# Optimization experiments

Hardware: AMD Instinct MI355X
Metric: run time of the kernel (lower is better)

Reference implementation:

```python
import jax, jax.numpy as jnp
import numpy as np

NUM_HEADS = 32
HEAD_DIM = 128
NUM_KV_HEADS = 8
SCALE = HEAD_DIM ** -0.5
BS = 2
SEQ_LEN = 2048


def setup_inputs() -> dict:
    key = jax.random.key(0)
    kq, kk, kv = jax.random.split(key, 3)
    q = jax.random.normal(kq, (BS * SEQ_LEN, NUM_HEADS * HEAD_DIM), dtype=jnp.float32)
    k = jax.random.normal(kk, (BS * SEQ_LEN, NUM_KV_HEADS * HEAD_DIM), dtype=jnp.float32)
    v = jax.random.normal(kv, (BS * SEQ_LEN, NUM_KV_HEADS * HEAD_DIM), dtype=jnp.float32)
    return {"q": q, "k": k, "v": v, "bs": BS, "seq_len": SEQ_LEN}


def reference(q, k, v, bs, seq_len):
    # Training-path: causal GQA attention (F.scaled_dot_product_attention, is_causal=True)
    qh = q.reshape(bs, seq_len, NUM_HEADS, HEAD_DIM)        # [b, s, h, d]
    kh = k.reshape(bs, seq_len, NUM_KV_HEADS, HEAD_DIM)     # [b, s, hk, d]
    vh = v.reshape(bs, seq_len, NUM_KV_HEADS, HEAD_DIM)
    rep = NUM_HEADS // NUM_KV_HEADS
    kh = jnp.repeat(kh, rep, axis=2)                         # [b, s, h, d]
    vh = jnp.repeat(vh, rep, axis=2)
    # scores [b, h, q, k]
    scores = jnp.einsum("bqhd,bkhd->bhqk", qh, kh) * SCALE
    causal = jnp.tril(jnp.ones((seq_len, seq_len), dtype=bool))
    scores = jnp.where(causal[None, None], scores, jnp.finfo(scores.dtype).min)
    probs = jax.nn.softmax(scores, axis=-1)
    o = jnp.einsum("bhqk,bkhd->bqhd", probs, vh)             # [b, q, h, d]
    return o.reshape(bs * seq_len, NUM_HEADS * HEAD_DIM)
```

## Files before the change

kernel.cpp:

```cpp
#include <hip/hip_runtime.h>

#define NUM_HEADS 32
#define HEAD_DIM 128
#define NUM_KV_HEADS 8
#define SEQ 2048
#define BATCH 2
#define BQ 128

typedef __attribute__((ext_vector_type(8))) short bf16x8;
typedef __attribute__((ext_vector_type(16))) float f32x16;
typedef __attribute__((ext_vector_type(4))) unsigned u32x4;

__device__ __forceinline__ short f2bf(float f) {
    unsigned u = __float_as_uint(f);
    u += 0x7fffu + ((u >> 16) & 1u);
    return (short)(u >> 16);
}
__device__ __forceinline__ unsigned pack2r(float a, float b) {
    unsigned ua = __float_as_uint(a) + 0x8000u;
    unsigned ub = __float_as_uint(b) + 0x8000u;
    return __builtin_amdgcn_perm(ub, ua, 0x07060302);
}
__device__ __forceinline__ float fexp2(float x) { return __builtin_amdgcn_exp2f(x); }

__global__ __launch_bounds__(256)
void conv_kv(const float* __restrict__ kg, const float* __restrict__ vg,
             short* __restrict__ kb, short* __restrict__ vt) {
    const int bid = blockIdx.x, tid = threadIdx.x;
    __shared__ float T[32][132];
    if (bid < 1024) {
        const float SL = 0.08838834764831845f * 1.4426950408889634f;
        int kvt = bid & 63, hk = (bid >> 6) & 7, b = bid >> 9;
#pragma unroll
        for (int i = 0; i < 4; ++i) {
            int slot = i * 256 + tid, row = slot >> 5, col = (slot & 31) * 4;
            float4 v = *(const float4*)(kg + ((size_t)(b * SEQ + kvt * 32 + row) * NUM_KV_HEADS + hk)
                                              * HEAD_DIM + col);
            *(float4*)&T[row][col] = v;
        }
        __syncthreads();
        short* dst = kb + (size_t)(b * NUM_KV_HEADS + hk) * SEQ * HEAD_DIM;
#pragma unroll
        for (int cc = 0; cc < 2; ++cc) {
            int c = tid * 2 + cc;
            int s = c >> 6, lane = c & 63, l32 = lane & 31, half = lane >> 5;
            float4 t0 = *(const float4*)&T[l32][s * 16 + half * 8];
            float4 t1 = *(const float4*)&T[l32][s * 16 + half * 8 + 4];
            bf16x8 o = { f2bf(t0.x * SL), f2bf(t0.y * SL), f2bf(t0.z * SL), f2bf(t0.w * SL),
                         f2bf(t1.x * SL), f2bf(t1.y * SL), f2bf(t1.z * SL), f2bf(t1.w * SL) };
            *(bf16x8*)(dst + ((size_t)(kvt * 8 + s) * 64 + lane) * 8) = o;
        }
    } else {
        int bidx = bid - 1024;
        int kvc = bidx & 63, hk = (bidx >> 6) & 7, b = bidx >> 9;
#pragma unroll
        for (int i = 0; i < 4; ++i) {
            int slot = i * 256 + tid, row = slot >> 5, col = (slot & 31) * 4;
            float4 v = *(const float4*)(vg + ((size_t)(b * SEQ + kvc * 32 + row) * NUM_KV_HEADS + hk)
                                              * HEAD_DIM + col);
            *(float4*)&T[row][col] = v;
        }
        __syncthreads();
        short* dst = vt + (size_t)(b * NUM_KV_HEADS + hk) * SEQ * HEAD_DIM;
#pragma unroll
        for (int cc = 0; cc < 2; ++cc) {
            int c = tid * 2 + cc;
            int chunk = c >> 6;
            int lane = c & 63, l32 = lane & 31, half = lane >> 5;
            int dtile = chunk >> 1, kk = chunk & 1;
            bf16x8 o;
#pragma unroll
            for (int j = 0; j < 8; ++j) o[j] = f2bf(T[kk * 16 + half * 8 + j][dtile * 32 + l32]);
            *(bf16x8*)(dst + ((size_t)(kvc * 8 + chunk) * 64 + lane) * 8) = o;
        }
    }
}

template<bool MASK>
__device__ __forceinline__ void kv_step(const short* __restrict__ Ks,
                                        const short* __restrict__ Vs,
                                        const bf16x8 (&qf)[8], f32x16 (&o)[4],
                                        float& rls, int l32, int half, int lane) {
    f32x16 s4;
#pragma unroll
    for (int r = 0; r < 16; ++r) s4[r] = 0.f;
#pragma unroll
    for (int h2 = 0; h2 < 2; ++h2) {
        bf16x8 kf[4];
#pragma unroll
        for (int s = 0; s < 4; ++s)
            kf[s] = *(const bf16x8*)(Ks + ((h2 * 4 + s) << 9) + lane * 8);
#pragma unroll
        for (int s = 0; s < 4; ++s)
            s4 = __builtin_amdgcn_mfma_f32_32x32x16_bf16(kf[s], qf[h2 * 4 + s], s4, 0, 0, 0);
    }

    if (MASK) {
#pragma unroll
        for (int r = 0; r < 16; ++r) {
            int klocal = (r & 3) + 8 * (r >> 2) + 4 * half;
            s4[r] = (klocal <= l32) ? s4[r] : -1e30f;
        }
    }

#pragma unroll
    for (int r = 0; r < 16; ++r) s4[r] = fexp2(s4[r]);

    {
        float t0 = (s4[0] + s4[1]) + (s4[2] + s4[3]);
        float t1 = (s4[4] + s4[5]) + (s4[6] + s4[7]);
        float t2 = (s4[8] + s4[9]) + (s4[10] + s4[11]);
        float t3 = (s4[12] + s4[13]) + (s4[14] + s4[15]);
        rls += (t0 + t1) + (t2 + t3);
    }

    unsigned p0 = pack2r(s4[0],  s4[1]);
    unsigned p1 = pack2r(s4[2],  s4[3]);
    unsigned p2 = pack2r(s4[4],  s4[5]);
    unsigned p3 = pack2r(s4[6],  s4[7]);
    unsigned p4 = pack2r(s4[8],  s4[9]);
    unsigned p5 = pack2r(s4[10], s4[11]);
    unsigned p6 = pack2r(s4[12], s4[13]);
    unsigned p7 = pack2r(s4[14], s4[15]);
    unsigned t0 = half ? p0 : p2;
    unsigned t1 = half ? p1 : p3;
    unsigned t2 = half ? p4 : p6;
    unsigned t3 = half ? p5 : p7;
    unsigned u0 = (unsigned)__shfl_xor((int)t0, 32);
    unsigned u1 = (unsigned)__shfl_xor((int)t1, 32);
    unsigned u2 = (unsigned)__shfl_xor((int)t2, 32);
    unsigned u3 = (unsigned)__shfl_xor((int)t3, 32);
    u32x4 w0 = { half ? u0 : p0, half ? u1 : p1, half ? p2 : u0, half ? p3 : u1 };
    u32x4 w1 = { half ? u2 : p4, half ? u3 : p5, half ? p6 : u2, half ? p7 : u3 };
    bf16x8 pf0 = __builtin_bit_cast(bf16x8, w0);
    bf16x8 pf1 = __builtin_bit_cast(bf16x8, w1);

#pragma unroll
    for (int h2 = 0; h2 < 2; ++h2) {
        bf16x8 vf[4];
#pragma unroll
        for (int c = 0; c < 4; ++c)
            vf[c] = *(const bf16x8*)(Vs + ((h2 * 4 + c) << 9) + lane * 8);
#pragma unroll
        for (int c = 0; c < 4; ++c) {
            int cg = h2 * 4 + c;
            o[cg >> 1] = __builtin_amdgcn_mfma_f32_32x32x16_bf16(
                vf[c], (cg & 1) ? pf1 : pf0, o[cg >> 1], 0, 0, 0);
        }
    }
}

__global__ __launch_bounds__(256, 3)
void fattn_kernel(const float* __restrict__ qg, const short* __restrict__ kb,
                  const short* __restrict__ vt, float* __restrict__ outg) {
    __shared__ short sh[2][8192];

    const int tid  = threadIdx.x;
    const int wave = tid >> 6;
    const int lane = tid & 63;
    const int l32  = lane & 31;
    const int half = lane >> 5;

    const int bid  = (int)blockIdx.x;
    const int hk   = bid & 7;
    const int rest = bid >> 3;
    const int b    = rest & 1;
    const int hj   = (rest >> 1) & 3;
    const int qt   = 15 - (rest >> 3);
    const int h    = hk * 4 + hj;

    const int q0w = qt * BQ + wave * 32;

    bf16x8 qf[8];
    {
        const float* qp = qg + (size_t)(b * SEQ + q0w + l32) * (NUM_HEADS * HEAD_DIM)
                             + h * HEAD_DIM + half * 8;
#pragma unroll
        for (int s = 0; s < 8; ++s) {
            float4 a = *(const float4*)(qp + s * 16);
            float4 c = *(const float4*)(qp + s * 16 + 4);
            bf16x8 f = { f2bf(a.x), f2bf(a.y), f2bf(a.z), f2bf(a.w),
                         f2bf(c.x), f2bf(c.y), f2bf(c.z), f2bf(c.w) };
            qf[s] = f;
        }
    }

    const short* kreg = kb + (size_t)(b * NUM_KV_HEADS + hk) * SEQ * HEAD_DIM;
    const short* vreg = vt + (size_t)(b * NUM_KV_HEADS + hk) * SEQ * HEAD_DIM;

    f32x16 o[4];
#pragma unroll
    for (int dt = 0; dt < 4; ++dt)
#pragma unroll
        for (int r = 0; r < 16; ++r) o[dt][r] = 0.f;
    float rls = 0.f;

    const int nblk = 4 * qt + 4;
    const int nfw  = 4 * qt + wave;

#define STAGE(ktn, bf_)                                                           \
    {                                                                             \
        const short* ksrc_ = kreg + ((size_t)(ktn) << 12) + lane * 8;             \
        const short* vsrc_ = vreg + ((size_t)(ktn) << 12) + lane * 8;             \
        _Pragma("unroll")                                                         \
        for (int i_ = 0; i_ < 4; ++i_) {                                          \
            int ch_ = wave * 4 + i_;                                              \
            const short* g_ = (ch_ < 8) ? (ksrc_ + (ch_ << 9))                    \
                                        : (vsrc_ + ((ch_ - 8) << 9));             \
            __builtin_amdgcn_global_load_lds(                                     \
                (const __attribute__((address_space(1))) void*)g_,                \
                (__attribute__((address_space(3))) void*)&sh[bf_][ch_ << 9],      \
                16, 0, 0);                                                        \
        }                                                                         \
    }

    STAGE(0, 0);
    __syncthreads();

    int cur = 0;
    for (int kt = 0; kt < nblk; ++kt) {
        if (kt + 1 < nblk) STAGE(kt + 1, cur ^ 1);
        if (kt < nfw)
            kv_step<false>(&sh[cur][0], &sh[cur][4096], qf, o, rls, l32, half, lane);
        else if (kt == nfw)
            kv_step<true>(&sh[cur][0], &sh[cur][4096], qf, o, rls, l32, half, lane);
        __syncthreads();
        cur ^= 1;
    }
#undef STAGE

    const float rl = rls + __shfl_xor(rls, 32);
    const float inv = 1.0f / rl;

    float* op = outg + (size_t)(b * SEQ + q0w + l32) * (NUM_HEADS * HEAD_DIM) + h * HEAD_DIM;
#pragma unroll
    for (int dt = 0; dt < 4; ++dt)
#pragma unroll
        for (int blk = 0; blk < 4; ++blk) {
            float4 w = { o[dt][4 * blk + 0] * inv, o[dt][4 * blk + 1] * inv,
                         o[dt][4 * blk + 2] * inv, o[dt][4 * blk + 3] * inv };
            *(float4*)(op + dt * 32 + blk * 8 + half * 4) = w;
        }
}

extern "C" void kernel_launch(void* const* d_in, const int* in_sizes, int n_in,
                              void* d_out, int out_size, void* d_ws, size_t ws_size,
                              hipStream_t stream) {
    const float* q = (const float*)d_in[0];
    const float* k = (const float*)d_in[1];
    const float* v = (const float*)d_in[2];
    float* out = (float*)d_out;

    short* kbuf  = (short*)d_ws;
    short* vtbuf = kbuf + (size_t)BATCH * NUM_KV_HEADS * SEQ * HEAD_DIM;

    conv_kv<<<2048, 256, 0, stream>>>(k, v, kbuf, vtbuf);
    fattn_kernel<<<dim3(1024), dim3(256), 0, stream>>>(q, kbuf, vtbuf, out);
}
```

Before: 219.0 us.

## Double query rows per wave to reuse each K/V tile across two Q blocks

Each wave now processes two 32-row query blocks (BQ 256), so K and V fragments loaded from LDS are reused for two score and two PV MFMA chains. The grid halves to 512 blocks, and query tiles are ordered so the first half runs heavy tiles first and the second half light ones, for load balance. This doubles accumulator and Q registers, so launch bounds drop to 2 blocks per CU, and fewer blocks means coarser causal imbalance.

```diff
diff --git a/kernel.cpp b/kernel.cpp
--- a/kernel.cpp
+++ b/kernel.cpp
@@ -5,7 +5,7 @@
 #define NUM_KV_HEADS 8
 #define SEQ 2048
 #define BATCH 2
-#define BQ 128
+#define BQ 256
 
 typedef __attribute__((ext_vector_type(8))) short bf16x8;
 typedef __attribute__((ext_vector_type(16))) float f32x16;
@@ -76,36 +76,10 @@
     }
 }
 
-template<bool MASK>
-__device__ __forceinline__ void kv_step(const short* __restrict__ Ks,
-                                        const short* __restrict__ Vs,
-                                        const bf16x8 (&qf)[8], f32x16 (&o)[4],
-                                        float& rls, int l32, int half, int lane) {
-    f32x16 s4;
-#pragma unroll
-    for (int r = 0; r < 16; ++r) s4[r] = 0.f;
-#pragma unroll
-    for (int h2 = 0; h2 < 2; ++h2) {
-        bf16x8 kf[4];
-#pragma unroll
-        for (int s = 0; s < 4; ++s)
-            kf[s] = *(const bf16x8*)(Ks + ((h2 * 4 + s) << 9) + lane * 8);
-#pragma unroll
-        for (int s = 0; s < 4; ++s)
-            s4 = __builtin_amdgcn_mfma_f32_32x32x16_bf16(kf[s], qf[h2 * 4 + s], s4, 0, 0, 0);
-    }
-
-    if (MASK) {
-#pragma unroll
-        for (int r = 0; r < 16; ++r) {
-            int klocal = (r & 3) + 8 * (r >> 2) + 4 * half;
-            s4[r] = (klocal <= l32) ? s4[r] : -1e30f;
-        }
-    }
-
+__device__ __forceinline__ void sm_pack(f32x16& s4, float& rls, int half,
+                                        bf16x8& pfa, bf16x8& pfb) {
 #pragma unroll
     for (int r = 0; r < 16; ++r) s4[r] = fexp2(s4[r]);
-
     {
         float t0 = (s4[0] + s4[1]) + (s4[2] + s4[3]);
         float t1 = (s4[4] + s4[5]) + (s4[6] + s4[7]);
@@ -113,7 +87,6 @@
         float t3 = (s4[12] + s4[13]) + (s4[14] + s4[15]);
         rls += (t0 + t1) + (t2 + t3);
     }
-
     unsigned p0 = pack2r(s4[0],  s4[1]);
     unsigned p1 = pack2r(s4[2],  s4[3]);
     unsigned p2 = pack2r(s4[4],  s4[5]);
@@ -132,8 +105,55 @@
     unsigned u3 = (unsigned)__shfl_xor((int)t3, 32);
     u32x4 w0 = { half ? u0 : p0, half ? u1 : p1, half ? p2 : u0, half ? p3 : u1 };
     u32x4 w1 = { half ? u2 : p4, half ? u3 : p5, half ? p6 : u2, half ? p7 : u3 };
-    bf16x8 pf0 = __builtin_bit_cast(bf16x8, w0);
-    bf16x8 pf1 = __builtin_bit_cast(bf16x8, w1);
+    pfa = __builtin_bit_cast(bf16x8, w0);
+    pfb = __builtin_bit_cast(bf16x8, w1);
+}
+
+template<bool DO0, bool M0, bool M1>
+__device__ __forceinline__ void kv_step2(const short* __restrict__ Ks,
+                                         const short* __restrict__ Vs,
+                                         const bf16x8 (&qfA)[8], const bf16x8 (&qfB)[8],
+                                         f32x16 (&o0)[4], f32x16 (&o1)[4],
+                                         float& rls0, float& rls1,
+                                         int l32, int half, int lane) {
+    bf16x8 kf[8];
+#pragma unroll
+    for (int s = 0; s < 8; ++s)
+        kf[s] = *(const bf16x8*)(Ks + (s << 9) + lane * 8);
+
+    bf16x8 pf0a, pf0b, pf1a, pf1b;
+    if (DO0) {
+        f32x16 s4;
+#pragma unroll
+        for (int r = 0; r < 16; ++r) s4[r] = 0.f;
+#pragma unroll
+        for (int s = 0; s < 8; ++s)
+            s4 = __builtin_amdgcn_mfma_f32_32x32x16_bf16(kf[s], qfA[s], s4, 0, 0, 0);
+        if (M0) {
+#pragma unroll
+            for (int r = 0; r < 16; ++r) {
+                int klocal = (r & 3) + 8 * (r >> 2) + 4 * half;
+                s4[r] = (klocal <= l32) ? s4[r] : -1e30f;
+            }
+        }
+        sm_pack(s4, rls0, half, pf0a, pf0b);
+    }
+    {
+        f32x16 s4;
+#pragma unroll
+        for (int r = 0; r < 16; ++r) s4[r] = 0.f;
+#pragma unroll
+        for (int s = 0; s < 8; ++s)
+            s4 = __builtin_amdgcn_mfma_f32_32x32x16_bf16(kf[s], qfB[s], s4, 0, 0, 0);
+        if (M1) {
+#pragma unroll
+            for (int r = 0; r < 16; ++r) {
+                int klocal = (r & 3) + 8 * (r >> 2) + 4 * half;
+                s4[r] = (klocal <= l32) ? s4[r] : -1e30f;
+            }
+        }
+        sm_pack(s4, rls1, half, pf1a, pf1b);
+    }
 
 #pragma unroll
     for (int h2 = 0; h2 < 2; ++h2) {
@@ -143,14 +163,17 @@
             vf[c] = *(const bf16x8*)(Vs + ((h2 * 4 + c) << 9) + lane * 8);
 #pragma unroll
         for (int c = 0; c < 4; ++c) {
-            int cg = h2 * 4 + c;
-            o[cg >> 1] = __builtin_amdgcn_mfma_f32_32x32x16_bf16(
-                vf[c], (cg & 1) ? pf1 : pf0, o[cg >> 1], 0, 0, 0);
-        }
-    }
-}
-
-__global__ __launch_bounds__(256, 3)
+            int cg = h2 * 4 + c, dt = cg >> 1;
+            if (DO0)
+                o0[dt] = __builtin_amdgcn_mfma_f32_32x32x16_bf16(
+                    vf[c], (cg & 1) ? pf0b : pf0a, o0[dt], 0, 0, 0);
+            o1[dt] = __builtin_amdgcn_mfma_f32_32x32x16_bf16(
+                vf[c], (cg & 1) ? pf1b : pf1a, o1[dt], 0, 0, 0);
+        }
+    }
+}
+
+__global__ __launch_bounds__(256, 2)
 void fattn_kernel(const float* __restrict__ qg, const short* __restrict__ kb,
                   const short* __restrict__ vt, float* __restrict__ outg) {
     __shared__ short sh[2][8192];
@@ -164,16 +187,19 @@
     const int bid  = (int)blockIdx.x;
     const int hk   = bid & 7;
     const int rest = bid >> 3;
-    const int b    = rest & 1;
-    const int hj   = (rest >> 1) & 3;
-    const int qt   = 15 - (rest >> 3);
+    const int j    = rest & 31;
+    const int b    = j & 1;
+    const int hj   = (j >> 1) & 3;
+    const int qi   = j >> 3;
+    const int qt   = (rest < 32) ? (7 - qi) : qi;
     const int h    = hk * 4 + hj;
 
-    const int q0w = qt * BQ + wave * 32;
-
-    bf16x8 qf[8];
-    {
-        const float* qp = qg + (size_t)(b * SEQ + q0w + l32) * (NUM_HEADS * HEAD_DIM)
+    const int q0w = qt * BQ + wave * 64;
+
+    bf16x8 qfA[8], qfB[8];
+#pragma unroll
+    for (int qb = 0; qb < 2; ++qb) {
+        const float* qp = qg + (size_t)(b * SEQ + q0w + qb * 32 + l32) * (NUM_HEADS * HEAD_DIM)
                              + h * HEAD_DIM + half * 8;
 #pragma unroll
         for (int s = 0; s < 8; ++s) {
@@ -181,22 +207,22 @@
             float4 c = *(const float4*)(qp + s * 16 + 4);
             bf16x8 f = { f2bf(a.x), f2bf(a.y), f2bf(a.z), f2bf(a.w),
                          f2bf(c.x), f2bf(c.y), f2bf(c.z), f2bf(c.w) };
-            qf[s] = f;
+            if (qb == 0) qfA[s] = f; else qfB[s] = f;
         }
     }
 
     const short* kreg = kb + (size_t)(b * NUM_KV_HEADS + hk) * SEQ * HEAD_DIM;
     const short* vreg = vt + (size_t)(b * NUM_KV_HEADS + hk) * SEQ * HEAD_DIM;
 
-    f32x16 o[4];
+    f32x16 o0[4], o1[4];
 #pragma unroll
     for (int dt = 0; dt < 4; ++dt)
 #pragma unroll
-        for (int r = 0; r < 16; ++r) o[dt][r] = 0.f;
-    float rls = 0.f;
-
-    const int nblk = 4 * qt + 4;
-    const int nfw  = 4 * qt + wave;
+        for (int r = 0; r < 16; ++r) { o0[dt][r] = 0.f; o1[dt][r] = 0.f; }
+    float rls0 = 0.f, rls1 = 0.f;
+
+    const int nblk  = 8 * qt + 8;
+    const int diag0 = 8 * qt + 2 * wave;
 
 #define STAGE(ktn, bf_)                                                           \
     {                                                                             \
@@ -220,27 +246,39 @@
     int cur = 0;
     for (int kt = 0; kt < nblk; ++kt) {
         if (kt + 1 < nblk) STAGE(kt + 1, cur ^ 1);
-        if (kt < nfw)
-            kv_step<false>(&sh[cur][0], &sh[cur][4096], qf, o, rls, l32, half, lane);
-        else if (kt == nfw)
-            kv_step<true>(&sh[cur][0], &sh[cur][4096], qf, o, rls, l32, half, lane);
+        const short* Ks = &sh[cur][0];
+        const short* Vs = &sh[cur][4096];
+        if (kt < diag0)
+            kv_step2<true, false, false>(Ks, Vs, qfA, qfB, o0, o1, rls0, rls1, l32, half, lane);
+        else if (kt == diag0)
+            kv_step2<true, true, false>(Ks, Vs, qfA, qfB, o0, o1, rls0, rls1, l32, half, lane);
+        else if (kt == diag0 + 1)
+            kv_step2<false, false, true>(Ks, Vs, qfA, qfB, o0, o1, rls0, rls1, l32, half, lane);
         __syncthreads();
         cur ^= 1;
     }
 #undef STAGE
 
-    const float rl = rls + __shfl_xor(rls, 32);
-    const float inv = 1.0f / rl;
-
-    float* op = outg + (size_t)(b * SEQ + q0w + l32) * (NUM_HEADS * HEAD_DIM) + h * HEAD_DIM;
-#pragma unroll
-    for (int dt = 0; dt < 4; ++dt)
-#pragma unroll
-        for (int blk = 0; blk < 4; ++blk) {
-            float4 w = { o[dt][4 * blk + 0] * inv, o[dt][4 * blk + 1] * inv,
-                         o[dt][4 * blk + 2] * inv, o[dt][4 * blk + 3] * inv };
-            *(float4*)(op + dt * 32 + blk * 8 + half * 4) = w;
-        }
+    const float rl0 = rls0 + __shfl_xor(rls0, 32);
+    const float rl1 = rls1 + __shfl_xor(rls1, 32);
+    const float inv0 = 1.0f / rl0;
+    const float inv1 = 1.0f / rl1;
+
+#pragma unroll
+    for (int qb = 0; qb < 2; ++qb) {
+        const float inv = qb ? inv1 : inv0;
+        float* op = outg + (size_t)(b * SEQ + q0w + qb * 32 + l32) * (NUM_HEADS * HEAD_DIM)
+                         + h * HEAD_DIM;
+#pragma unroll
+        for (int dt = 0; dt < 4; ++dt)
+#pragma unroll
+            for (int blk = 0; blk < 4; ++blk) {
+                const f32x16& oo = qb ? o1[dt] : o0[dt];
+                float4 w = { oo[4 * blk + 0] * inv, oo[4 * blk + 1] * inv,
+                             oo[4 * blk + 2] * inv, oo[4 * blk + 3] * inv };
+                *(float4*)(op + dt * 32 + blk * 8 + half * 4) = w;
+            }
+    }
 }
 
 extern "C" void kernel_launch(void* const* d_in, const int* in_sizes, int n_in,
@@ -255,5 +293,5 @@
     short* vtbuf = kbuf + (size_t)BATCH * NUM_KV_HEADS * SEQ * HEAD_DIM;
 
     conv_kv<<<2048, 256, 0, stream>>>(k, v, kbuf, vtbuf);
-    fattn_kernel<<<dim3(1024), dim3(256), 0, stream>>>(q, kbuf, vtbuf, out);
-}
+    fattn_kernel<<<dim3(512), dim3(256), 0, stream>>>(q, kbuf, vtbuf, out);
+}
```

Result: slower. 254.8 us (+16.3%).
